# Kernel tuning notes

Hardware: AMD Instinct MI355X
Metric: run time of the kernel (lower is better)

The kernel has to match this reference:

```python
import jax, jax.numpy as jnp
import numpy as np

D_K = 64
N_HEADS = 12
LN_EPS = 1e-5


def layer_norm(x, eps=LN_EPS):
    # nn.LayerNorm(768) is created fresh each forward -> weight=1, bias=0
    mu = jnp.mean(x, axis=-1, keepdims=True)
    var = jnp.mean(jnp.square(x - mu), axis=-1, keepdims=True)
    return (x - mu) * jax.lax.rsqrt(var + eps)


def setup_inputs() -> dict:
    key = jax.random.key(0)
    ks = jax.random.split(key, 7)
    B, S, D = 2, 2048, 768
    scale = 1.0 / np.sqrt(D)
    return {
        "input_Q": jax.random.normal(ks[0], (B, S, D), jnp.float32),
        "input_K": jax.random.normal(ks[1], (B, S, D), jnp.float32),
        "input_V": jax.random.normal(ks[2], (B, S, D), jnp.float32),
        "Wq": jax.random.normal(ks[3], (D, D), jnp.float32) * scale,
        "Wk": jax.random.normal(ks[4], (D, D), jnp.float32) * scale,
        "Wv": jax.random.normal(ks[5], (D, D), jnp.float32) * scale,
        "Wo": jax.random.normal(ks[6], (D, D), jnp.float32) * scale,
    }


def reference(input_Q, input_K, input_V, Wq, Wk, Wv, Wo):
    B, Sq, D = input_Q.shape
    Sk = input_K.shape[1]
    H, dk = N_HEADS, D_K
    residual = input_Q
    # projections: [B,S,D] @ [D, H*dk] -> [B,H,S,dk]
    Q = (input_Q @ Wq).reshape(B, Sq, H, dk).transpose(0, 2, 1, 3)
    K = (input_K @ Wk).reshape(B, Sk, H, dk).transpose(0, 2, 1, 3)
    V = (input_V @ Wv).reshape(B, Sk, H, dk).transpose(0, 2, 1, 3)
    # attention scores [B,H,Sq,Sk]
    att = jnp.einsum("bhqd,bhkd->bhqk", Q, K) / np.sqrt(dk).astype(np.float32)
    att = jax.nn.softmax(att, axis=-1)
    ctx = jnp.einsum("bhqk,bhkd->bhqd", att, V)  # [B,H,Sq,dk]
    ctx = ctx.transpose(0, 2, 1, 3).reshape(B, Sq, H * dk)
    out = ctx @ Wo
    return layer_norm(out + residual)
```

## Files before the change

### kernel.cpp

```cpp
#include <hip/hip_runtime.h>
#include <hip/hip_bf16.h>
#include <stdint.h>

#define S_LEN 2048
#define D_MODEL 768
#define NH 12
#define DK 64
#define BATCH 2
#define M_TOT (BATCH * S_LEN)

typedef __attribute__((ext_vector_type(8))) short short8;
typedef __attribute__((ext_vector_type(4))) float f32x4;
typedef __attribute__((ext_vector_type(16))) float f32x16;

__device__ inline short f2bf(float f) {
  union { float f; uint32_t u; } v; v.f = f;
  uint32_t r = v.u + 0x7fffu + ((v.u >> 16) & 1u);
  return (short)(r >> 16);
}

__device__ inline f32x4 mfma16(short8 a, short8 b, f32x4 c) {
  return __builtin_amdgcn_mfma_f32_16x16x32_bf16(a, b, c, 0, 0, 0);
}
__device__ inline f32x16 mfma32(short8 a, short8 b, f32x16 c) {
  return __builtin_amdgcn_mfma_f32_32x32x16_bf16(a, b, c, 0, 0, 0);
}

__device__ inline void gl16(const void* g, void* l) {
  __builtin_amdgcn_global_load_lds(
      (const __attribute__((address_space(1))) unsigned*)g,
      (__attribute__((address_space(3))) unsigned*)l, 16, 0, 0);
}

__device__ inline unsigned cvtpk(float lo, float hi) {
  unsigned r;
  asm("v_cvt_pk_bf16_f32 %0, %1, %2" : "=v"(r) : "v"(lo), "v"(hi));
  return r;
}
__device__ inline void plswap(unsigned& a, unsigned& b) {
  asm("v_permlane32_swap_b32 %0, %1" : "+v"(a), "+v"(b));
}

__global__ __launch_bounds__(256) void transpose_w_kernel(
    const float* __restrict__ Wq, const float* __restrict__ Wk,
    const float* __restrict__ Wv, const float* __restrict__ Wo,
    short* __restrict__ WT) {
  int z = blockIdx.z;
  const float* W = z == 0 ? Wq : (z == 1 ? Wk : (z == 2 ? Wv : Wo));
  short* O = WT + (size_t)z * D_MODEL * D_MODEL;
  __shared__ float t[32][33];
  int x = threadIdx.x, y = threadIdx.y;
  int nb = blockIdx.x * 32, kb = blockIdx.y * 32;
#pragma unroll
  for (int j = 0; j < 4; ++j)
    t[y + 8 * j][x] = W[(kb + y + 8 * j) * D_MODEL + nb + x];
  __syncthreads();
#pragma unroll
  for (int j = 0; j < 4; ++j)
    O[(nb + y + 8 * j) * D_MODEL + kb + x] = f2bf(t[x][y + 8 * j]);
}

__global__ __launch_bounds__(256) void cast_x_kernel(
    const float* __restrict__ Xq, const float* __restrict__ Xk,
    const float* __restrict__ Xv, short* __restrict__ Xb) {
  int z = blockIdx.y;
  const float* X = z == 0 ? Xq : (z == 1 ? Xk : Xv);
  short* O = Xb + (size_t)z * M_TOT * D_MODEL;
  size_t i = ((size_t)blockIdx.x * 256 + threadIdx.x) * 8;
  float4 f0 = *(const float4*)(X + i);
  float4 f1 = *(const float4*)(X + i + 4);
  short8 v;
  v[0] = f2bf(f0.x); v[1] = f2bf(f0.y); v[2] = f2bf(f0.z); v[3] = f2bf(f0.w);
  v[4] = f2bf(f1.x); v[5] = f2bf(f1.y); v[6] = f2bf(f1.z); v[7] = f2bf(f1.w);
  *(short8*)(O + i) = v;
}

__global__ __launch_bounds__(256) void proj_kernel(
    const short* __restrict__ Xb, const short* __restrict__ WTall,
    short* __restrict__ Qo, short* __restrict__ Ko, short* __restrict__ Vo) {
  int bid = blockIdx.x;
  int wk = (bid & 7) * 72 + (bid >> 3);
  int which = wk / 192;
  int rem = wk % 192;
  int mt = rem / 6, nt = rem % 6;
  int mbase = mt * 128, nbase = nt * 128;
  const short* X = Xb + (size_t)which * M_TOT * D_MODEL;
  const short* WT = WTall + (size_t)which * D_MODEL * D_MODEL;

  __shared__ short As[128][32];
  __shared__ short Bs[128][32];
  int tid = threadIdx.x;
  int wv = tid >> 6, lane = tid & 63, r = lane & 15, g = lane >> 4;
  int wm = (wv & 1) * 64, wn = (wv >> 1) * 64;
  int srow = (lane >> 2), scol = (lane & 3) * 8;

  f32x4 acc[4][4] = {};
  for (int kk = 0; kk < D_MODEL; kk += 32) {
#pragma unroll
    for (int j = 0; j < 2; ++j) {
      int row = wv * 32 + j * 16;
      gl16(X + (size_t)(mbase + row + srow) * D_MODEL + kk + scol, &As[row][0]);
      gl16(WT + (size_t)(nbase + row + srow) * D_MODEL + kk + scol, &Bs[row][0]);
    }
    __syncthreads();
    short8 a[4], b[4];
#pragma unroll
    for (int i = 0; i < 4; ++i) {
      a[i] = *(short8*)&As[wm + i * 16 + r][g * 8];
      b[i] = *(short8*)&Bs[wn + i * 16 + r][g * 8];
    }
#pragma unroll
    for (int i = 0; i < 4; ++i)
#pragma unroll
      for (int j = 0; j < 4; ++j)
        acc[i][j] = mfma16(a[i], b[j], acc[i][j]);
    __syncthreads();
  }
#pragma unroll
  for (int i = 0; i < 4; ++i)
#pragma unroll
    for (int j = 0; j < 4; ++j)
#pragma unroll
      for (int reg = 0; reg < 4; ++reg) {
        int m = mbase + wm + i * 16 + g * 4 + reg;
        int n = nbase + wn + j * 16 + r;
        int b_ = m >> 11, s = m & 2047, h = n >> 6, d = n & 63;
        if (which == 0) {
          short v = f2bf(acc[i][j][reg] * 0.18033688f);
          Qo[(((size_t)b_ * NH + h) * S_LEN + s) * DK + d] = v;
        } else if (which == 1) {
          short v = f2bf(acc[i][j][reg]);
          Ko[(((size_t)b_ * NH + h) * S_LEN + s) * DK + (d ^ ((s & 7) << 3))] = v;
        } else {
          short v = f2bf(acc[i][j][reg]);
          Vo[(((size_t)b_ * NH + h) * DK + d) * S_LEN + (s ^ ((d & 7) << 3))] = v;
        }
      }
}

__global__ __launch_bounds__(128) void attn_kernel(
    const short* __restrict__ Qg, const short* __restrict__ Kg,
    const short* __restrict__ Vt, short* __restrict__ ctx) {
  __shared__ char K_lds[2][8192];
  __shared__ char V_lds[2][8192];
  int bh = blockIdx.y;
  int b = bh / NH, h = bh % NH;
  int tid = threadIdx.x;
  int w = tid >> 6, lane = tid & 63;
  int c32 = lane & 31, hi = lane >> 5;
  int qbase = blockIdx.x * 64 + w * 32;
  const short* qp = Qg + (size_t)bh * S_LEN * DK;
  const char* kp = (const char*)(Kg + (size_t)bh * S_LEN * DK);
  const char* vp = (const char*)(Vt + (size_t)bh * DK * S_LEN);

  short8 qf[4];
#pragma unroll
  for (int kk = 0; kk < 4; ++kk)
    qf[kk] = *(const short8*)(qp + (size_t)(qbase + c32) * DK + kk * 16 + hi * 8);

#define STAGE(buf, kc)                                                          \
  {                                                                             \
    _Pragma("unroll") for (int j = 0; j < 4; ++j) {                             \
      int p = w * 4 + j;                                                        \
      gl16(kp + (size_t)(kc)*128 + p * 1024 + lane * 16, &K_lds[buf][p * 1024]);\
    }                                                                           \
    _Pragma("unroll") for (int j = 0; j < 4; ++j) {                             \
      int p = w * 4 + j;                                                        \
      int row = p * 8 + (lane >> 3);                                            \
      gl16(vp + (size_t)row * 4096 + (kc)*2 + (lane & 7) * 16,                  \
           &V_lds[buf][p * 1024]);                                              \
    }                                                                           \
  }

  STAGE(0, 0);

  f32x16 o0 = {}, o1 = {};
  float m_run = -30000.f, l_run = 0.f;
  int cur = 0;

  for (int t = 0; t < S_LEN / 64; ++t) {
    if (t < S_LEN / 64 - 1) {
      STAGE(cur ^ 1, (t + 1) * 64);
      asm volatile("s_waitcnt vmcnt(8)" ::: "memory");
    } else {
      asm volatile("s_waitcnt vmcnt(0)" ::: "memory");
    }
    __builtin_amdgcn_s_barrier();

    const char* kb = K_lds[cur];
    const char* vb = V_lds[cur];

    f32x16 st0 = {}, st1 = {};
#pragma unroll
    for (int kk = 0; kk < 4; ++kk) {
      int cb = kk * 32 + hi * 16;
      short8 k0 = *(const short8*)(kb + c32 * 128 + (cb ^ ((c32 & 7) << 4)));
      short8 k1 = *(const short8*)(kb + (32 + c32) * 128 + (cb ^ ((c32 & 7) << 4)));
      st0 = mfma32(k0, qf[kk], st0);
      st1 = mfma32(k1, qf[kk], st1);
    }

    float cm = -30000.f;
#pragma unroll
    for (int i = 0; i < 16; ++i) cm = fmaxf(cm, fmaxf(st0[i], st1[i]));
    cm = fmaxf(cm, __shfl_xor(cm, 32));
    if (!__all(cm <= m_run + 8.0f)) {
      float m_new = fmaxf(m_run, cm);
      float al = __builtin_amdgcn_exp2f(m_run - m_new);
      l_run *= al;
      m_run = m_new;
#pragma unroll
      for (int r = 0; r < 16; ++r) {
        int ql = (r & 3) + 8 * (r >> 2) + 4 * hi;
        float ar = __shfl(al, ql);
        o0[r] *= ar;
        o1[r] *= ar;
      }
    }
    float csum = 0.f;
#pragma unroll
    for (int i = 0; i < 16; ++i) {
      st0[i] = __builtin_amdgcn_exp2f(st0[i] - m_run);
      st1[i] = __builtin_amdgcn_exp2f(st1[i] - m_run);
      csum += st0[i] + st1[i];
    }
    csum += __shfl_xor(csum, 32);
    l_run += csum;

#pragma unroll
    for (int ks = 0; ks < 4; ++ks) {
      f32x16 P = (ks < 2) ? st0 : st1;
      int s8 = (ks & 1) * 8;
      unsigned A = cvtpk(P[s8 + 0], P[s8 + 1]);
      unsigned Bx = cvtpk(P[s8 + 4], P[s8 + 5]);
      unsigned C = cvtpk(P[s8 + 2], P[s8 + 3]);
      unsigned Dx = cvtpk(P[s8 + 6], P[s8 + 7]);
      plswap(A, Bx);
      plswap(C, Dx);
      union { unsigned u[4]; short8 s; } pu;
      pu.u[0] = A; pu.u[1] = C; pu.u[2] = Bx; pu.u[3] = Dx;
      int cb = ks * 32 + hi * 16;
      short8 v0 = *(const short8*)(vb + c32 * 128 + (cb ^ ((c32 & 7) << 4)));
      short8 v1 = *(const short8*)(vb + (32 + c32) * 128 + (cb ^ ((c32 & 7) << 4)));
      o0 = mfma32(pu.s, v0, o0);
      o1 = mfma32(pu.s, v1, o1);
    }

    __builtin_amdgcn_s_barrier();
    cur ^= 1;
  }

  size_t rowbase = (size_t)b * S_LEN + qbase;
#pragma unroll
  for (int r = 0; r < 16; ++r) {
    int ql = (r & 3) + 8 * (r >> 2) + 4 * hi;
    float linv = 1.0f / __shfl(l_run, ql);
    short* cp = ctx + (rowbase + ql) * D_MODEL + h * DK;
    cp[c32] = f2bf(o0[r] * linv);
    cp[32 + c32] = f2bf(o1[r] * linv);
  }
#undef STAGE
}

__global__ __launch_bounds__(256) void outln_kernel(
    const short* __restrict__ ctx, const short* __restrict__ WoT,
    const float* __restrict__ resid, float* __restrict__ out) {
  int mbase = blockIdx.x * 16;
  int tid = threadIdx.x;
  int w = tid >> 6, lane = tid & 63, r = lane & 15, g = lane >> 4;
  f32x4 acc[12] = {};
  for (int kk = 0; kk < D_MODEL; kk += 32) {
    short8 a = *(const short8*)(ctx + (size_t)(mbase + r) * D_MODEL + kk + g * 8);
#pragma unroll
    for (int j = 0; j < 12; ++j) {
      int n = w * 192 + j * 16 + r;
      short8 bv = *(const short8*)(WoT + (size_t)n * D_MODEL + kk + g * 8);
      acc[j] = mfma16(a, bv, acc[j]);
    }
  }
  __shared__ float redS[16][4];
  __shared__ float redQ[16][4];
  float ps[4], pq[4];
#pragma unroll
  for (int reg = 0; reg < 4; ++reg) {
    int m = mbase + g * 4 + reg;
    float s = 0.f, q = 0.f;
#pragma unroll
    for (int j = 0; j < 12; ++j) {
      float v = acc[j][reg] + resid[(size_t)m * D_MODEL + w * 192 + j * 16 + r];
      acc[j][reg] = v;
      s += v;
      q += v * v;
    }
    ps[reg] = s; pq[reg] = q;
  }
#pragma unroll
  for (int reg = 0; reg < 4; ++reg) {
    float s = ps[reg], q = pq[reg];
    s += __shfl_xor(s, 1); q += __shfl_xor(q, 1);
    s += __shfl_xor(s, 2); q += __shfl_xor(q, 2);
    s += __shfl_xor(s, 4); q += __shfl_xor(q, 4);
    s += __shfl_xor(s, 8); q += __shfl_xor(q, 8);
    if (r == 0) { redS[g * 4 + reg][w] = s; redQ[g * 4 + reg][w] = q; }
  }
  __syncthreads();
#pragma unroll
  for (int reg = 0; reg < 4; ++reg) {
    int row = g * 4 + reg;
    float s = redS[row][0] + redS[row][1] + redS[row][2] + redS[row][3];
    float q = redQ[row][0] + redQ[row][1] + redQ[row][2] + redQ[row][3];
    float mu = s * (1.0f / 768.0f);
    float var = q * (1.0f / 768.0f) - mu * mu;
    float rstd = rsqrtf(var + 1e-5f);
    int m = mbase + row;
#pragma unroll
    for (int j = 0; j < 12; ++j)
      out[(size_t)m * D_MODEL + w * 192 + j * 16 + r] = (acc[j][reg] - mu) * rstd;
  }
}

extern "C" void kernel_launch(void* const* d_in, const int* in_sizes, int n_in,
                              void* d_out, int out_size, void* d_ws, size_t ws_size,
                              hipStream_t stream) {
  const float* xq = (const float*)d_in[0];
  const float* xk = (const float*)d_in[1];
  const float* xv = (const float*)d_in[2];
  const float* Wq = (const float*)d_in[3];
  const float* Wk = (const float*)d_in[4];
  const float* Wv = (const float*)d_in[5];
  const float* Wo = (const float*)d_in[6];
  float* out = (float*)d_out;

  char* ws = (char*)d_ws;
  const size_t WSZ = (size_t)D_MODEL * D_MODEL;
  const size_t QSZ = (size_t)M_TOT * D_MODEL;
  short* WT = (short*)ws;
  short* Xb = WT + 4 * WSZ;
  short* Qb = Xb + 3 * QSZ;
  short* Kb = Qb + QSZ;
  short* Vb = Kb + QSZ;
  short* Cx = Vb + QSZ;

  transpose_w_kernel<<<dim3(24, 24, 4), dim3(32, 8), 0, stream>>>(Wq, Wk, Wv, Wo, WT);
  cast_x_kernel<<<dim3(1536, 3), 256, 0, stream>>>(xq, xk, xv, Xb);
  proj_kernel<<<576, 256, 0, stream>>>(Xb, WT, Qb, Kb, Vb);
  attn_kernel<<<dim3(32, 24), 128, 0, stream>>>(Qb, Kb, Vb, Cx);
  outln_kernel<<<dim3(256), 256, 0, stream>>>(Cx, WT + 3 * WSZ, xq, out);
}
```

Measured before the change: 269.5 us.

## Split output projection into LDS-tiled 128x128 GEMM plus separate LayerNorm kernel

Replaces the fused output-projection+LayerNorm kernel, which used 16-row blocks that reread Wo directly from global memory, with a 128x128 LDS-tiled GEMM that writes out+residual to a float scratch buffer. A separate row-wise LayerNorm kernel then normalizes it. The goal is much better reuse of Wo and ctx tiles. The cost is an extra launch and a full fp32 round trip through memory, and only 192 blocks fill the GPU.

```diff
diff --git a/kernel.cpp b/kernel.cpp
--- a/kernel.cpp
+++ b/kernel.cpp
@@ -262,61 +262,80 @@
 #undef STAGE
 }
 
-__global__ __launch_bounds__(256) void outln_kernel(
+__global__ __launch_bounds__(256) void gemm_out_kernel(
     const short* __restrict__ ctx, const short* __restrict__ WoT,
-    const float* __restrict__ resid, float* __restrict__ out) {
-  int mbase = blockIdx.x * 16;
+    const float* __restrict__ resid, float* __restrict__ Y) {
+  int bid = blockIdx.x;
+  int wk = (bid & 7) * 24 + (bid >> 3);
+  int mt = wk / 6, nt = wk % 6;
+  int mbase = mt * 128, nbase = nt * 128;
+
+  __shared__ short As[128][32];
+  __shared__ short Bs[128][32];
   int tid = threadIdx.x;
-  int w = tid >> 6, lane = tid & 63, r = lane & 15, g = lane >> 4;
-  f32x4 acc[12] = {};
+  int wv = tid >> 6, lane = tid & 63, r = lane & 15, g = lane >> 4;
+  int wm = (wv & 1) * 64, wn = (wv >> 1) * 64;
+  int srow = (lane >> 2), scol = (lane & 3) * 8;
+
+  f32x4 acc[4][4] = {};
   for (int kk = 0; kk < D_MODEL; kk += 32) {
-    short8 a = *(const short8*)(ctx + (size_t)(mbase + r) * D_MODEL + kk + g * 8);
-#pragma unroll
-    for (int j = 0; j < 12; ++j) {
-      int n = w * 192 + j * 16 + r;
-      short8 bv = *(const short8*)(WoT + (size_t)n * D_MODEL + kk + g * 8);
-      acc[j] = mfma16(a, bv, acc[j]);
-    }
-  }
-  __shared__ float redS[16][4];
-  __shared__ float redQ[16][4];
-  float ps[4], pq[4];
-#pragma unroll
-  for (int reg = 0; reg < 4; ++reg) {
-    int m = mbase + g * 4 + reg;
-    float s = 0.f, q = 0.f;
-#pragma unroll
-    for (int j = 0; j < 12; ++j) {
-      float v = acc[j][reg] + resid[(size_t)m * D_MODEL + w * 192 + j * 16 + r];
-      acc[j][reg] = v;
-      s += v;
-      q += v * v;
-    }
-    ps[reg] = s; pq[reg] = q;
-  }
-#pragma unroll
-  for (int reg = 0; reg < 4; ++reg) {
-    float s = ps[reg], q = pq[reg];
-    s += __shfl_xor(s, 1); q += __shfl_xor(q, 1);
-    s += __shfl_xor(s, 2); q += __shfl_xor(q, 2);
-    s += __shfl_xor(s, 4); q += __shfl_xor(q, 4);
-    s += __shfl_xor(s, 8); q += __shfl_xor(q, 8);
-    if (r == 0) { redS[g * 4 + reg][w] = s; redQ[g * 4 + reg][w] = q; }
-  }
-  __syncthreads();
-#pragma unroll
-  for (int reg = 0; reg < 4; ++reg) {
-    int row = g * 4 + reg;
-    float s = redS[row][0] + redS[row][1] + redS[row][2] + redS[row][3];
-    float q = redQ[row][0] + redQ[row][1] + redQ[row][2] + redQ[row][3];
-    float mu = s * (1.0f / 768.0f);
-    float var = q * (1.0f / 768.0f) - mu * mu;
-    float rstd = rsqrtf(var + 1e-5f);
-    int m = mbase + row;
-#pragma unroll
-    for (int j = 0; j < 12; ++j)
-      out[(size_t)m * D_MODEL + w * 192 + j * 16 + r] = (acc[j][reg] - mu) * rstd;
-  }
+#pragma unroll
+    for (int j = 0; j < 2; ++j) {
+      int row = wv * 32 + j * 16;
+      gl16(ctx + (size_t)(mbase + row + srow) * D_MODEL + kk + scol, &As[row][0]);
+      gl16(WoT + (size_t)(nbase + row + srow) * D_MODEL + kk + scol, &Bs[row][0]);
+    }
+    __syncthreads();
+    short8 a[4], b[4];
+#pragma unroll
+    for (int i = 0; i < 4; ++i) {
+      a[i] = *(short8*)&As[wm + i * 16 + r][g * 8];
+      b[i] = *(short8*)&Bs[wn + i * 16 + r][g * 8];
+    }
+#pragma unroll
+    for (int i = 0; i < 4; ++i)
+#pragma unroll
+      for (int j = 0; j < 4; ++j)
+        acc[i][j] = mfma16(a[i], b[j], acc[i][j]);
+    __syncthreads();
+  }
+#pragma unroll
+  for (int i = 0; i < 4; ++i)
+#pragma unroll
+    for (int j = 0; j < 4; ++j)
+#pragma unroll
+      for (int reg = 0; reg < 4; ++reg) {
+        int m = mbase + wm + i * 16 + g * 4 + reg;
+        int n = nbase + wn + j * 16 + r;
+        Y[(size_t)m * D_MODEL + n] = acc[i][j][reg] + resid[(size_t)m * D_MODEL + n];
+      }
+}
+
+__global__ __launch_bounds__(256) void ln_kernel(const float* __restrict__ Y,
+                                                 float* __restrict__ out) {
+  int row = blockIdx.x * 4 + (threadIdx.x >> 6);
+  int l = threadIdx.x & 63;
+  const float* yp = Y + (size_t)row * D_MODEL;
+  float v[12];
+  float s = 0.f, q = 0.f;
+#pragma unroll
+  for (int c = 0; c < 12; ++c) {
+    v[c] = yp[c * 64 + l];
+    s += v[c];
+    q += v[c] * v[c];
+  }
+#pragma unroll
+  for (int d = 1; d < 64; d <<= 1) {
+    s += __shfl_xor(s, d);
+    q += __shfl_xor(q, d);
+  }
+  float mu = s * (1.0f / 768.0f);
+  float var = q * (1.0f / 768.0f) - mu * mu;
+  float rstd = rsqrtf(var + 1e-5f);
+  float* op = out + (size_t)row * D_MODEL;
+#pragma unroll
+  for (int c = 0; c < 12; ++c)
+    op[c * 64 + l] = (v[c] - mu) * rstd;
 }
 
 extern "C" void kernel_launch(void* const* d_in, const int* in_sizes, int n_in,
@@ -340,10 +359,12 @@
   short* Kb = Qb + QSZ;
   short* Vb = Kb + QSZ;
   short* Cx = Vb + QSZ;
+  float* Yf = (float*)Xb;
 
   transpose_w_kernel<<<dim3(24, 24, 4), dim3(32, 8), 0, stream>>>(Wq, Wk, Wv, Wo, WT);
   cast_x_kernel<<<dim3(1536, 3), 256, 0, stream>>>(xq, xk, xv, Xb);
   proj_kernel<<<576, 256, 0, stream>>>(Xb, WT, Qb, Kb, Vb);
   attn_kernel<<<dim3(32, 24), 128, 0, stream>>>(Qb, Kb, Vb, Cx);
-  outln_kernel<<<dim3(256), 256, 0, stream>>>(Cx, WT + 3 * WSZ, xq, out);
-}
+  gemm_out_kernel<<<192, 256, 0, stream>>>(Cx, WT + 3 * WSZ, xq, Yf);
+  ln_kernel<<<1024, 256, 0, stream>>>(Yf, out);
+}
```

Measured after the change: 226.0 us. 1.19x faster.
